# Performance work log

Hardware: AMD Instinct MI355X
Metric: run time of the kernel (lower is better)

Reference implementation:

```python
import jax, jax.numpy as jnp
import numpy as np

N_LAYERS = 2
D_MODEL = 1024
D_INNER = 2 * D_MODEL
D_STATE = 16
D_CONV = 4
DT_RANK = D_MODEL // 16  # 64
B_SZ, L = 1, 2048
EPS = 1e-5


def layernorm(x, w, b):
    mu = jnp.mean(x, axis=-1, keepdims=True)
    var = jnp.mean(jnp.square(x - mu), axis=-1, keepdims=True)
    return (x - mu) * jax.lax.rsqrt(var + EPS) * w + b


def mamba(x, in_w, cw, cb, xp_w, dtp_w, dtp_b, A_log, Dp, out_w):
    # x: [B, L, D_MODEL]
    Bn, Ln, _ = x.shape
    xz = jnp.einsum('bld,ed->ble', x, in_w)          # [B,L,2*D_INNER]
    xc, z = jnp.split(xz, 2, axis=-1)
    # causal depthwise conv1d (kernel D_CONV)
    xp = jnp.pad(xc, ((0, 0), (D_CONV - 1, 0), (0, 0)))
    xc = sum(xp[:, k:k + Ln, :] * cw[:, k] for k in range(D_CONV)) + cb
    xc = jax.nn.silu(xc)
    dbl = jnp.einsum('ble,re->blr', xc, xp_w)        # [B,L,DT_RANK+2*D_STATE]
    dt, Bm, Cm = jnp.split(dbl, [DT_RANK, DT_RANK + D_STATE], axis=-1)
    dt = jax.nn.softplus(jnp.einsum('blr,er->ble', dt, dtp_w) + dtp_b)  # [B,L,E]
    A = -jnp.exp(A_log)                              # [E,N], strictly negative
    dA = jnp.exp(dt[..., None] * A)                  # [B,L,E,N]
    dBu = (dt * xc)[..., None] * Bm[:, :, None, :]   # [B,L,E,N]

    def step(h, inp):
        dA_t, dBu_t, C_t = inp
        h = dA_t * h + dBu_t                         # [B,E,N]
        y = jnp.einsum('ben,bn->be', h, C_t)
        return h, y

    h0 = jnp.zeros((Bn, D_INNER, D_STATE), dA.dtype)
    _, ys = jax.lax.scan(step, h0, (dA.transpose(1, 0, 2, 3),
                                    dBu.transpose(1, 0, 2, 3),
                                    Cm.transpose(1, 0, 2)))
    y = ys.transpose(1, 0, 2) + xc * Dp              # [B,L,E]
    y = y * jax.nn.silu(z)
    return jnp.einsum('ble,de->bld', y, out_w)       # [B,L,D_MODEL]


def setup_inputs() -> dict:
    key = jax.random.key(0)
    ks = jax.random.split(key, 12)
    s = 0.02
    dt_init = np.log(np.expm1(0.01)).astype(np.float32)  # softplus^-1(0.01)
    A_row = jnp.log(jnp.arange(1, D_STATE + 1, dtype=jnp.float32))
    return {
        'x': jax.random.normal(ks[0], (B_SZ, L, D_MODEL), jnp.float32),
        'ln_w': jnp.ones((N_LAYERS, D_MODEL), jnp.float32),
        'ln_b': jnp.zeros((N_LAYERS, D_MODEL), jnp.float32),
        'in_proj_w': jax.random.normal(ks[1], (N_LAYERS, 2 * D_INNER, D_MODEL)) * s,
        'conv_w': jax.random.normal(ks[2], (N_LAYERS, D_INNER, D_CONV)) * 0.2,
        'conv_b': jnp.zeros((N_LAYERS, D_INNER), jnp.float32),
        'x_proj_w': jax.random.normal(ks[3], (N_LAYERS, DT_RANK + 2 * D_STATE, D_INNER)) * s,
        'dt_proj_w': jax.random.normal(ks[4], (N_LAYERS, D_INNER, DT_RANK)) * (DT_RANK ** -0.5),
        'dt_proj_b': jnp.full((N_LAYERS, D_INNER), dt_init),
        'A_log': jnp.broadcast_to(A_row, (N_LAYERS, D_INNER, D_STATE)).copy(),
        'D_skip': jnp.ones((N_LAYERS, D_INNER), jnp.float32),
        'out_proj_w': jax.random.normal(ks[5], (N_LAYERS, D_MODEL, D_INNER)) * s,
        'norm_f_w': jnp.ones((D_MODEL,), jnp.float32),
        'norm_f_b': jnp.zeros((D_MODEL,), jnp.float32),
    }


def reference(x, ln_w, ln_b, in_proj_w, conv_w, conv_b, x_proj_w, dt_proj_w,
              dt_proj_b, A_log, D_skip, out_proj_w, norm_f_w, norm_f_b):
    for i in range(N_LAYERS):
        h = layernorm(x, ln_w[i], ln_b[i])
        h = mamba(h, in_proj_w[i], conv_w[i], conv_b[i], x_proj_w[i],
                  dt_proj_w[i], dt_proj_b[i], A_log[i], D_skip[i], out_proj_w[i])
        x = h + x  # residual (dropout/drop_path are identity in eval)
    return layernorm(x, norm_f_w, norm_f_b)
```

## Files before the change

kernel.cpp:

```cpp
#include <hip/hip_runtime.h>
#include <hip/hip_bf16.h>
#include <math.h>

#define LSEQ 2048
#define DMODEL 1024
#define DINNER 2048
#define DSTATE 16
#define DCONV 4
#define DTRANK 64
#define RPROJ 96

#define CHUNK 32
#define NCHUNK (LSEQ / CHUNK)

#define XSPLIT 4

typedef __attribute__((ext_vector_type(8))) short bf16x8;
typedef __attribute__((ext_vector_type(4))) float f32x4;

__device__ __forceinline__ float softplusf(float x) {
    return (x > 20.f) ? x : log1pf(__expf(x));
}
__device__ __forceinline__ float siluf(float x) {
    return x / (1.f + __expf(-x));
}
__device__ __forceinline__ short f2bf(float f) {
    union { float f; unsigned u; } v; v.f = f;
    unsigned r = v.u + 0x7FFFu + ((v.u >> 16) & 1u);
    return (short)(r >> 16);
}
__device__ __forceinline__ float bf2f(short h) {
    union { unsigned u; float f; } v;
    v.u = ((unsigned)(unsigned short)h) << 16;
    return v.f;
}

__device__ __forceinline__ void cvt8(const float* __restrict__ s,
                                     short* __restrict__ d, int i) {
    const float4 a = *(const float4*)(s + i);
    const float4 b = *(const float4*)(s + i + 4);
    alignas(16) short h[8];
    h[0] = f2bf(a.x); h[1] = f2bf(a.y); h[2] = f2bf(a.z); h[3] = f2bf(a.w);
    h[4] = f2bf(b.x); h[5] = f2bf(b.y); h[6] = f2bf(b.z); h[7] = f2bf(b.w);
    *(uint4*)(d + i) = *(const uint4*)h;
}

__device__ __forceinline__ void ln_phase(
    const float* __restrict__ x, const float* __restrict__ w,
    const float* __restrict__ b, float* __restrict__ outf,
    short* __restrict__ outb, int bid, int tid)
{
    const int wv = tid >> 6, lane = tid & 63;
    const int row = bid * 4 + wv;
    const float* xr = x + (size_t)row * DMODEL;
    float v[16];
    float s = 0.f, sq = 0.f;
#pragma unroll
    for (int k = 0; k < 16; k++) {
        v[k] = xr[k * 64 + lane];
        s += v[k];
        sq += v[k] * v[k];
    }
#pragma unroll
    for (int off = 32; off > 0; off >>= 1) {
        s += __shfl_xor(s, off, 64);
        sq += __shfl_xor(sq, off, 64);
    }
    const float mu = s * (1.f / DMODEL);
    const float var = sq * (1.f / DMODEL) - mu * mu;
    const float rstd = rsqrtf(var + 1e-5f);
#pragma unroll
    for (int k = 0; k < 16; k++) {
        const int i = k * 64 + lane;
        const float o = (v[k] - mu) * rstd * w[i] + b[i];
        if (outf) outf[(size_t)row * DMODEL + i] = o;
        else      outb[(size_t)row * DMODEL + i] = f2bf(o);
    }
}

__global__ __launch_bounds__(256) void cvt_ln_kernel(
    const float* __restrict__ in_w, short* __restrict__ in_w_bf,
    const float* __restrict__ xp_w, short* __restrict__ xp_w_bf,
    const float* __restrict__ out_w, short* __restrict__ out_w_bf,
    const float* __restrict__ dtp_w, short* __restrict__ dtp_w_bf,
    const float* __restrict__ x_in, const float* __restrict__ ln_w,
    const float* __restrict__ ln_b, short* __restrict__ h_bf)
{
    const int n1 = 2 * (2 * DINNER) * DMODEL;
    const int n2 = 2 * RPROJ * DINNER;
    const int n3 = 2 * DMODEL * DINNER;
    const int bid = blockIdx.x;
    const int tid = threadIdx.x;
    {
        int i = (bid * 256 + tid) * 8;
        if (i < n1) { cvt8(in_w, in_w_bf, i); goto done_cvt; }
        i -= n1;
        if (i < n2) { cvt8(xp_w, xp_w_bf, i); goto done_cvt; }
        i -= n2;
        if (i < n3) { cvt8(out_w, out_w_bf, i); goto done_cvt; }
        i -= n3;
        cvt8(dtp_w, dtp_w_bf, i);
    }
done_cvt:
    if (bid < LSEQ / 4)
        ln_phase(x_in, ln_w, ln_b, nullptr, h_bf, bid, tid);
}

__global__ __launch_bounds__(256) void ln_g(
    const float* __restrict__ x, const float* __restrict__ w,
    const float* __restrict__ b, float* __restrict__ outf,
    short* __restrict__ outb)
{
    ln_phase(x, w, b, outf, outb, blockIdx.x, threadIdx.x);
}

template<int MI, int NJ, int MODE>
__global__ __launch_bounds__(256) void gemm_g(
    const short* __restrict__ A, int lda,
    const short* __restrict__ W, int ldw,
    float* __restrict__ Cf, short* __restrict__ Cb, int ldc,
    int N, int K, const float* __restrict__ resid)
{
    constexpr int BM = 32 * MI;
    constexpr int BN = 32 * NJ;
    constexpr int AISS = BM / 32;
    constexpr int WISS = BN / 32;
    __shared__ alignas(16) short As[BM * 64];
    __shared__ alignas(16) short Ws[BN * 64];

    const int tid = threadIdx.x;
    const int lane = tid & 63;
    const int w = tid >> 6;
    const int wr = w >> 1, wc = w & 1;
    const int row0 = blockIdx.y * BM;
    const int col0 = blockIdx.x * BN;
    const int kbeg = blockIdx.z * K;

    const int srow = tid >> 3;
    const int dch  = tid & 7;
    const int skch = (dch ^ (srow & 7)) * 8;

    f32x4 acc[MI][NJ];
#pragma unroll
    for (int i = 0; i < MI; i++)
#pragma unroll
        for (int j = 0; j < NJ; j++) acc[i][j] = (f32x4)0.f;

    const int lrow = lane & 15;
    const int q = lane >> 4;

    for (int kt = kbeg; kt < kbeg + K; kt += 64) {
        __syncthreads();
#pragma unroll
        for (int j = 0; j < AISS; j++) {
            const short* gp = A + (size_t)(row0 + j * 32 + srow) * lda + kt + skch;
            __builtin_amdgcn_global_load_lds(
                (const __attribute__((address_space(1))) void*)gp,
                (__attribute__((address_space(3))) void*)(&As[j * 2048 + tid * 8]),
                16, 0, 0);
        }
#pragma unroll
        for (int j = 0; j < WISS; j++) {
            const int wrow = col0 + j * 32 + srow;
            if (wrow < N) {
                const short* gp = W + (size_t)wrow * ldw + kt + skch;
                __builtin_amdgcn_global_load_lds(
                    (const __attribute__((address_space(1))) void*)gp,
                    (__attribute__((address_space(3))) void*)(&Ws[j * 2048 + tid * 8]),
                    16, 0, 0);
            }
        }
        __syncthreads();

#pragma unroll
        for (int ks = 0; ks < 2; ks++) {
            bf16x8 af[MI], bfr[NJ];
#pragma unroll
            for (int i = 0; i < MI; i++) {
                const int R = wr * (16 * MI) + i * 16 + lrow;
                const int pc = (ks * 4 + q) ^ (R & 7);
                af[i] = *(const bf16x8*)&As[R * 64 + pc * 8];
            }
#pragma unroll
            for (int j = 0; j < NJ; j++) {
                const int R = wc * (16 * NJ) + j * 16 + lrow;
                const int pc = (ks * 4 + q) ^ (R & 7);
                bfr[j] = *(const bf16x8*)&Ws[R * 64 + pc * 8];
            }
#pragma unroll
            for (int i = 0; i < MI; i++)
#pragma unroll
                for (int j = 0; j < NJ; j++)
                    acc[i][j] = __builtin_amdgcn_mfma_f32_16x16x32_bf16(
                        af[i], bfr[j], acc[i][j], 0, 0, 0);
        }
    }

    const int rbase = row0 + wr * (16 * MI);
    const int cbase = col0 + wc * (16 * NJ);
#pragma unroll
    for (int i = 0; i < MI; i++) {
#pragma unroll
        for (int j = 0; j < NJ; j++) {
            const int gcol = cbase + j * 16 + lrow;
            if (gcol < N) {
#pragma unroll
                for (int r = 0; r < 4; r++) {
                    const int grow = rbase + i * 16 + (lane >> 4) * 4 + r;
                    float v = acc[i][j][r];
                    if (MODE == 2) {
                        Cf[(size_t)grow * ldc + gcol] =
                            v + resid[(size_t)grow * ldc + gcol];
                    } else if (MODE == 3) {
                        Cb[(size_t)grow * ldc + gcol] = f2bf(v);
                    } else {
                        atomicAdd(&Cf[(size_t)grow * ldc + gcol], v);
                    }
                }
            }
        }
    }
}

__global__ __launch_bounds__(256) void dtproj_g(
    const float* __restrict__ dbl,
    const short* __restrict__ dtp_w,
    const float* __restrict__ dtp_b,
    short* __restrict__ dt_bf)
{
    __shared__ alignas(16) short As[64 * 32];
    __shared__ alignas(16) short Ws[128 * 32];
    const int tid = threadIdx.x;
    const int lane = tid & 63;
    const int w = tid >> 6;
    const int wr = w >> 1, wc = w & 1;
    const int row0 = blockIdx.y * 64;
    const int col0 = blockIdx.x * 128;
    const int srow = tid >> 2;
    const int skch = ((tid & 3) ^ ((srow >> 1) & 3)) * 8;
    const int lrow = lane & 15;
    const int q = lane >> 4;

    f32x4 acc[2][4];
#pragma unroll
    for (int i = 0; i < 2; i++)
#pragma unroll
        for (int j = 0; j < 4; j++) acc[i][j] = (f32x4)0.f;

#pragma unroll
    for (int kt = 0; kt < 64; kt += 32) {
        __syncthreads();
        {
            const float* gp = dbl + (size_t)(row0 + srow) * RPROJ + kt + skch;
            const float4 a = *(const float4*)gp;
            const float4 b = *(const float4*)(gp + 4);
            alignas(16) short h[8];
            h[0] = f2bf(a.x); h[1] = f2bf(a.y); h[2] = f2bf(a.z); h[3] = f2bf(a.w);
            h[4] = f2bf(b.x); h[5] = f2bf(b.y); h[6] = f2bf(b.z); h[7] = f2bf(b.w);
            *(uint4*)(As + tid * 8) = *(const uint4*)h;
        }
#pragma unroll
        for (int j = 0; j < 2; j++) {
            const short* gp = dtp_w + (size_t)(col0 + j * 64 + srow) * DTRANK + kt + skch;
            __builtin_amdgcn_global_load_lds(
                (const __attribute__((address_space(1))) void*)gp,
                (__attribute__((address_space(3))) void*)(&Ws[j * 2048 + tid * 8]),
                16, 0, 0);
        }
        __syncthreads();

        bf16x8 af[2], bfr[4];
#pragma unroll
        for (int i = 0; i < 2; i++) {
            const int R = wr * 32 + i * 16 + lrow;
            af[i] = *(const bf16x8*)&As[R * 32 + ((q ^ ((R >> 1) & 3)) * 8)];
        }
#pragma unroll
        for (int j = 0; j < 4; j++) {
            const int R = wc * 64 + j * 16 + lrow;
            bfr[j] = *(const bf16x8*)&Ws[R * 32 + ((q ^ ((R >> 1) & 3)) * 8)];
        }
#pragma unroll
        for (int i = 0; i < 2; i++)
#pragma unroll
            for (int j = 0; j < 4; j++)
                acc[i][j] = __builtin_amdgcn_mfma_f32_16x16x32_bf16(
                    af[i], bfr[j], acc[i][j], 0, 0, 0);
    }

    const int rbase = row0 + wr * 32;
    const int cbase = col0 + wc * 64;
#pragma unroll
    for (int i = 0; i < 2; i++)
#pragma unroll
        for (int j = 0; j < 4; j++) {
            const int gcol = cbase + j * 16 + lrow;
#pragma unroll
            for (int r = 0; r < 4; r++) {
                const int grow = rbase + i * 16 + (lane >> 4) * 4 + r;
                dt_bf[(size_t)grow * DINNER + gcol] =
                    f2bf(softplusf(acc[i][j][r] + dtp_b[gcol]));
            }
        }
}

__global__ __launch_bounds__(256) void conv_g(
    const short* __restrict__ xzb, const float* __restrict__ cw,
    const float* __restrict__ cb, short* __restrict__ xcb,
    float* __restrict__ dbl_zero)
{
    const int g = blockIdx.x * 256 + threadIdx.x;
    if (g < (LSEQ * RPROJ) / 4)
        *(float4*)(dbl_zero + g * 4) = make_float4(0.f, 0.f, 0.f, 0.f);
    const int t = g >> 8;
    const int c0 = (g & 255) * 8;
    float acc[8];
#pragma unroll
    for (int j = 0; j < 8; j++) acc[j] = cb[c0 + j];
#pragma unroll
    for (int k = 0; k < DCONV; k++) {
        const int tt = t - (DCONV - 1) + k;
        if (tt >= 0) {
            const bf16x8 v = *(const bf16x8*)(xzb + (size_t)tt * (2 * DINNER) + c0);
#pragma unroll
            for (int j = 0; j < 8; j++)
                acc[j] += bf2f(v[j]) * cw[(c0 + j) * DCONV + k];
        }
    }
    alignas(16) short h[8];
#pragma unroll
    for (int j = 0; j < 8; j++) h[j] = f2bf(siluf(acc[j]));
    *(uint4*)(xcb + (size_t)t * DINNER + c0) = *(const uint4*)h;
}

__global__ __launch_bounds__(256) void scan1_g(
    const short* __restrict__ dtb,
    const short* __restrict__ xcb,
    const float* __restrict__ dbl,
    const float* __restrict__ A_log,
    float* __restrict__ S,
    float* __restrict__ sumdt)
{
    const int e = blockIdx.x * 256 + threadIdx.x;
    const int c = blockIdx.y;
    float a[DSTATE];
#pragma unroll
    for (int n = 0; n < DSTATE; n++) a[n] = -__expf(A_log[(size_t)e * DSTATE + n]);
    float h[DSTATE];
#pragma unroll
    for (int n = 0; n < DSTATE; n++) h[n] = 0.f;
    float sd = 0.f;

    __shared__ float sBC[CHUNK][32];
    for (int i = threadIdx.x; i < CHUNK * 32; i += 256) {
        const int tl = i >> 5, j = i & 31;
        sBC[tl][j] = dbl[(size_t)(c * CHUNK + tl) * RPROJ + DTRANK + j];
    }
    __syncthreads();

    const size_t rb = (size_t)c * CHUNK * DINNER + e;
    short dt_c = dtb[rb], xc_c = xcb[rb];
#pragma unroll 4
    for (int tl = 0; tl < CHUNK; tl++) {
        short dt_n = 0, xc_n = 0;
        if (tl + 1 < CHUNK) {
            dt_n = dtb[rb + (size_t)(tl + 1) * DINNER];
            xc_n = xcb[rb + (size_t)(tl + 1) * DINNER];
        }
        const float dtv = bf2f(dt_c);
        const float du = dtv * bf2f(xc_c);
        sd += dtv;
#pragma unroll
        for (int n = 0; n < DSTATE; n++) {
            const float dA = __expf(dtv * a[n]);
            h[n] = dA * h[n] + du * sBC[tl][n];
        }
        dt_c = dt_n; xc_c = xc_n;
    }
    sumdt[(size_t)c * DINNER + e] = sd;
#pragma unroll
    for (int n = 0; n < DSTATE; n++)
        S[((size_t)c * DSTATE + n) * DINNER + e] = h[n];
}

__global__ __launch_bounds__(256) void scan2_g(
    const float* __restrict__ A_log,
    const float* __restrict__ sumdt,
    float* __restrict__ S)
{
    const int idx = blockIdx.x * 256 + threadIdx.x;
    const int e = idx & (DINNER - 1);
    const int n = idx >> 11;
    const float a = -__expf(A_log[(size_t)e * DSTATE + n]);
    const size_t base = (size_t)n * DINNER + e;
    const size_t cstr = (size_t)DSTATE * DINNER;
    float H = 0.f;
    for (int c = 0; c < NCHUNK; c += 4) {
        const float sc0 = S[base + (size_t)(c + 0) * cstr];
        const float sc1 = S[base + (size_t)(c + 1) * cstr];
        const float sc2 = S[base + (size_t)(c + 2) * cstr];
        const float sc3 = S[base + (size_t)(c + 3) * cstr];
        const float sd0 = sumdt[(size_t)(c + 0) * DINNER + e];
        const float sd1 = sumdt[(size_t)(c + 1) * DINNER + e];
        const float sd2 = sumdt[(size_t)(c + 2) * DINNER + e];
        const float sd3 = sumdt[(size_t)(c + 3) * DINNER + e];
        S[base + (size_t)(c + 0) * cstr] = H;
        H = __expf(a * sd0) * H + sc0;
        S[base + (size_t)(c + 1) * cstr] = H;
        H = __expf(a * sd1) * H + sc1;
        S[base + (size_t)(c + 2) * cstr] = H;
        H = __expf(a * sd2) * H + sc2;
        S[base + (size_t)(c + 3) * cstr] = H;
        H = __expf(a * sd3) * H + sc3;
    }
}

__global__ __launch_bounds__(256) void scan3_g(
    const short* __restrict__ dtb,
    const short* __restrict__ xcb,
    const float* __restrict__ dbl,
    const short* __restrict__ xzb,
    const float* __restrict__ A_log,
    const float* __restrict__ Dp,
    const float* __restrict__ S,
    short* __restrict__ yb)
{
    const int e = blockIdx.x * 256 + threadIdx.x;
    const int c = blockIdx.y;
    float a[DSTATE];
#pragma unroll
    for (int n = 0; n < DSTATE; n++) a[n] = -__expf(A_log[(size_t)e * DSTATE + n]);
    float h[DSTATE];
#pragma unroll
    for (int n = 0; n < DSTATE; n++)
        h[n] = S[((size_t)c * DSTATE + n) * DINNER + e];
    const float dskip = Dp[e];

    __shared__ float sBC[CHUNK][32];
    for (int i = threadIdx.x; i < CHUNK * 32; i += 256) {
        const int tl = i >> 5, j = i & 31;
        sBC[tl][j] = dbl[(size_t)(c * CHUNK + tl) * RPROJ + DTRANK + j];
    }
    __syncthreads();

    const size_t rb = (size_t)c * CHUNK * DINNER + e;
    const size_t zb = (size_t)c * CHUNK * (2 * DINNER) + DINNER + e;
    short dt_c = dtb[rb], xc_c = xcb[rb], z_c = xzb[zb];
#pragma unroll 4
    for (int tl = 0; tl < CHUNK; tl++) {
        short dt_n = 0, xc_n = 0, z_n = 0;
        if (tl + 1 < CHUNK) {
            dt_n = dtb[rb + (size_t)(tl + 1) * DINNER];
            xc_n = xcb[rb + (size_t)(tl + 1) * DINNER];
            z_n = xzb[zb + (size_t)(tl + 1) * (2 * DINNER)];
        }
        const float dtv = bf2f(dt_c);
        const float xcv = bf2f(xc_c);
        const float du = dtv * xcv;
        float yv = 0.f;
#pragma unroll
        for (int n = 0; n < DSTATE; n++) {
            const float dA = __expf(dtv * a[n]);
            h[n] = dA * h[n] + du * sBC[tl][n];
            yv += h[n] * sBC[tl][16 + n];
        }
        yv = (yv + xcv * dskip) * siluf(bf2f(z_c));
        yb[rb + (size_t)tl * DINNER] = f2bf(yv);
        dt_c = dt_n; xc_c = xc_n; z_c = z_n;
    }
}

extern "C" void kernel_launch(void* const* d_in, const int* in_sizes, int n_in,
                              void* d_out, int out_size, void* d_ws, size_t ws_size,
                              hipStream_t stream) {
    const float* x_in   = (const float*)d_in[0];
    const float* ln_w   = (const float*)d_in[1];
    const float* ln_b   = (const float*)d_in[2];
    const float* in_w   = (const float*)d_in[3];
    const float* conv_w = (const float*)d_in[4];
    const float* conv_b = (const float*)d_in[5];
    const float* xp_w   = (const float*)d_in[6];
    const float* dtp_w  = (const float*)d_in[7];
    const float* dtp_b  = (const float*)d_in[8];
    const float* A_log  = (const float*)d_in[9];
    const float* D_skip = (const float*)d_in[10];
    const float* out_w  = (const float*)d_in[11];
    const float* nf_w   = (const float*)d_in[12];
    const float* nf_b   = (const float*)d_in[13];
    float* out = (float*)d_out;

    float* w = (float*)d_ws;
    float* buf_x = w; w += (size_t)LSEQ * DMODEL;
    float* dbl   = w; w += (size_t)LSEQ * RPROJ;
    float* Sbuf  = w; w += (size_t)NCHUNK * DSTATE * DINNER;
    float* sumdt = w; w += (size_t)NCHUNK * DINNER;
    short* h_bf    = (short*)w; w += (size_t)LSEQ * DMODEL / 2;
    short* xz_bf   = (short*)w; w += (size_t)LSEQ * 2 * DINNER / 2;
    short* xc_bf   = (short*)w; w += (size_t)LSEQ * DINNER / 2;
    short* dt_bf   = (short*)w; w += (size_t)LSEQ * DINNER / 2;
    short* y_bf    = (short*)w; w += (size_t)LSEQ * DINNER / 2;
    short* in_w_bf  = (short*)w; w += (size_t)2 * (2 * DINNER) * DMODEL / 2;
    short* xp_w_bf  = (short*)w; w += (size_t)2 * RPROJ * DINNER / 2;
    short* dtp_w_bf = (short*)w; w += (size_t)2 * DINNER * DTRANK / 2;
    short* out_w_bf = (short*)w; w += (size_t)2 * DMODEL * DINNER / 2;

    {
        const int total = 2 * (2 * DINNER) * DMODEL + 2 * RPROJ * DINNER
                        + 2 * DMODEL * DINNER + 2 * DINNER * DTRANK;
        cvt_ln_kernel<<<dim3(total / (256 * 8)), dim3(256), 0, stream>>>(
            in_w, in_w_bf, xp_w, xp_w_bf, out_w, out_w_bf, dtp_w, dtp_w_bf,
            x_in, ln_w, ln_b, h_bf);
    }

    for (int layer = 0; layer < 2; layer++) {
        const float* resid_src = (layer == 0) ? x_in : buf_x;
        if (layer > 0)
            ln_g<<<dim3(LSEQ / 4), dim3(256), 0, stream>>>(
                resid_src, ln_w + layer * DMODEL, ln_b + layer * DMODEL,
                nullptr, h_bf);
        gemm_g<4, 4, 3><<<dim3((2 * DINNER) / 128, LSEQ / 128), dim3(256), 0, stream>>>(
            h_bf, DMODEL, in_w_bf + (size_t)layer * 2 * DINNER * DMODEL, DMODEL,
            nullptr, xz_bf, 2 * DINNER, 2 * DINNER, DMODEL, nullptr);
        conv_g<<<dim3((LSEQ * DINNER / 8) / 256), dim3(256), 0, stream>>>(
            xz_bf, conv_w + (size_t)layer * DINNER * DCONV, conv_b + layer * DINNER,
            xc_bf, dbl);
        gemm_g<2, 2, 6><<<dim3(2, LSEQ / 64, XSPLIT), dim3(256), 0, stream>>>(
            xc_bf, DINNER, xp_w_bf + (size_t)layer * RPROJ * DINNER, DINNER,
            dbl, nullptr, RPROJ, RPROJ, DINNER / XSPLIT, nullptr);
        dtproj_g<<<dim3(DINNER / 128, LSEQ / 64), dim3(256), 0, stream>>>(
            dbl, dtp_w_bf + (size_t)layer * DINNER * DTRANK,
            dtp_b + layer * DINNER, dt_bf);
        const float* Al = A_log + (size_t)layer * DINNER * DSTATE;
        scan1_g<<<dim3(DINNER / 256, NCHUNK), dim3(256), 0, stream>>>(
            dt_bf, xc_bf, dbl, Al, Sbuf, sumdt);
        scan2_g<<<dim3((DINNER * DSTATE) / 256), dim3(256), 0, stream>>>(
            Al, sumdt, Sbuf);
        scan3_g<<<dim3(DINNER / 256, NCHUNK), dim3(256), 0, stream>>>(
            dt_bf, xc_bf, dbl, xz_bf, Al, D_skip + layer * DINNER, Sbuf, y_bf);
        gemm_g<4, 2, 2><<<dim3(DMODEL / 64, LSEQ / 128), dim3(256), 0, stream>>>(
            y_bf, DINNER, out_w_bf + (size_t)layer * DMODEL * DINNER, DINNER,
            buf_x, nullptr, DMODEL, DMODEL, DINNER, resid_src);
    }
    ln_g<<<dim3(LSEQ / 4), dim3(256), 0, stream>>>(buf_x, nf_w, nf_b, out, nullptr);
}
```

Baseline: 476.1 us.

## Fuse causal conv+SiLU into x_proj GEMM and scans, drop xc buffer

Removes the standalone conv kernel and the xc_bf intermediate. The conv+SiLU is recomputed on the fly while staging the A tile of a new split-K x_proj GEMM, and again in both scan kernels from a sliding window over xz. Zeroing of the dbl accumulator moves into the in_proj GEMM epilogue, and CHUNK drops from 32 to 16, doubling scan parallelism at the cost of a larger chunk-state pass. The trade is redundant conv arithmetic and an extra kernel argument path in exchange for one fewer launch and less global traffic.

```diff
diff --git a/kernel.cpp b/kernel.cpp
--- a/kernel.cpp
+++ b/kernel.cpp
@@ -10,10 +10,11 @@
 #define DTRANK 64
 #define RPROJ 96
 
-#define CHUNK 32
+#define CHUNK 16
 #define NCHUNK (LSEQ / CHUNK)
 
 #define XSPLIT 4
+#define XKS (DINNER / XSPLIT)
 
 typedef __attribute__((ext_vector_type(8))) short bf16x8;
 typedef __attribute__((ext_vector_type(4))) float f32x4;
@@ -119,7 +120,8 @@
     const short* __restrict__ A, int lda,
     const short* __restrict__ W, int ldw,
     float* __restrict__ Cf, short* __restrict__ Cb, int ldc,
-    int N, int K, const float* __restrict__ resid)
+    int N, int K, const float* __restrict__ resid,
+    float* __restrict__ zbuf, int zcount4)
 {
     constexpr int BM = 32 * MI;
     constexpr int BN = 32 * NJ;
@@ -134,7 +136,6 @@
     const int wr = w >> 1, wc = w & 1;
     const int row0 = blockIdx.y * BM;
     const int col0 = blockIdx.x * BN;
-    const int kbeg = blockIdx.z * K;
 
     const int srow = tid >> 3;
     const int dch  = tid & 7;
@@ -149,7 +150,7 @@
     const int lrow = lane & 15;
     const int q = lane >> 4;
 
-    for (int kt = kbeg; kt < kbeg + K; kt += 64) {
+    for (int kt = 0; kt < K; kt += 64) {
         __syncthreads();
 #pragma unroll
         for (int j = 0; j < AISS; j++) {
@@ -211,15 +212,136 @@
                     if (MODE == 2) {
                         Cf[(size_t)grow * ldc + gcol] =
                             v + resid[(size_t)grow * ldc + gcol];
-                    } else if (MODE == 3) {
+                    } else {
                         Cb[(size_t)grow * ldc + gcol] = f2bf(v);
-                    } else {
-                        atomicAdd(&Cf[(size_t)grow * ldc + gcol], v);
                     }
                 }
             }
         }
     }
+    if (zbuf) {
+        const int g = (blockIdx.y * gridDim.x + blockIdx.x) * 256 + tid;
+        if (g < zcount4)
+            *(float4*)(zbuf + (size_t)g * 4) = make_float4(0.f, 0.f, 0.f, 0.f);
+    }
+}
+
+__global__ __launch_bounds__(256) void xproj_conv_g(
+    const short* __restrict__ xzb,
+    const float* __restrict__ cw,
+    const float* __restrict__ cb,
+    const short* __restrict__ W,
+    float* __restrict__ dbl)
+{
+    __shared__ alignas(16) short As[64 * 64];
+    __shared__ alignas(16) short Ws[64 * 64];
+    __shared__ float cw4[XKS][4];
+    __shared__ float cbl[XKS];
+
+    const int tid = threadIdx.x;
+    const int lane = tid & 63;
+    const int w = tid >> 6;
+    const int wr = w >> 1, wc = w & 1;
+    const int row0 = blockIdx.y * 64;
+    const int col0 = blockIdx.x * 64;
+    const int kbeg = blockIdx.z * XKS;
+    const int srow = tid >> 3;
+    const int dch  = tid & 7;
+    const int skch = (dch ^ (srow & 7)) * 8;
+    const int lrow = lane & 15;
+    const int q = lane >> 4;
+
+    {
+        const float4* cwsrc = (const float4*)cw;
+        *(float4*)&cw4[tid * 2][0]     = cwsrc[kbeg + tid * 2];
+        *(float4*)&cw4[tid * 2 + 1][0] = cwsrc[kbeg + tid * 2 + 1];
+        cbl[tid]       = cb[kbeg + tid];
+        cbl[tid + 256] = cb[kbeg + tid + 256];
+    }
+
+    f32x4 acc[2][2];
+#pragma unroll
+    for (int i = 0; i < 2; i++)
+#pragma unroll
+        for (int j = 0; j < 2; j++) acc[i][j] = (f32x4)0.f;
+
+    for (int kt = kbeg; kt < kbeg + XKS; kt += 64) {
+        __syncthreads();
+#pragma unroll
+        for (int j = 0; j < 2; j++) {
+            const int t = row0 + j * 32 + srow;
+            const int ch0 = kt + skch;
+            const int lc = ch0 - kbeg;
+            float a8[8];
+#pragma unroll
+            for (int i = 0; i < 8; i++) a8[i] = cbl[lc + i];
+#pragma unroll
+            for (int k = 0; k < DCONV; k++) {
+                const int tt = t - (DCONV - 1) + k;
+                if (tt >= 0) {
+                    const bf16x8 v = *(const bf16x8*)(xzb + (size_t)tt * (2 * DINNER) + ch0);
+#pragma unroll
+                    for (int i = 0; i < 8; i++)
+                        a8[i] += bf2f(v[i]) * cw4[lc + i][k];
+                }
+            }
+            alignas(16) short h8[8];
+#pragma unroll
+            for (int i = 0; i < 8; i++) h8[i] = f2bf(siluf(a8[i]));
+            *(uint4*)(&As[j * 2048 + tid * 8]) = *(const uint4*)h8;
+        }
+#pragma unroll
+        for (int j = 0; j < 2; j++) {
+            const int wrow = col0 + j * 32 + srow;
+            if (wrow < RPROJ) {
+                const short* gp = W + (size_t)wrow * DINNER + kt + skch;
+                __builtin_amdgcn_global_load_lds(
+                    (const __attribute__((address_space(1))) void*)gp,
+                    (__attribute__((address_space(3))) void*)(&Ws[j * 2048 + tid * 8]),
+                    16, 0, 0);
+            }
+        }
+        __syncthreads();
+
+#pragma unroll
+        for (int ks = 0; ks < 2; ks++) {
+            bf16x8 af[2], bfr[2];
+#pragma unroll
+            for (int i = 0; i < 2; i++) {
+                const int R = wr * 32 + i * 16 + lrow;
+                const int pc = (ks * 4 + q) ^ (R & 7);
+                af[i] = *(const bf16x8*)&As[R * 64 + pc * 8];
+            }
+#pragma unroll
+            for (int j = 0; j < 2; j++) {
+                const int R = wc * 32 + j * 16 + lrow;
+                const int pc = (ks * 4 + q) ^ (R & 7);
+                bfr[j] = *(const bf16x8*)&Ws[R * 64 + pc * 8];
+            }
+#pragma unroll
+            for (int i = 0; i < 2; i++)
+#pragma unroll
+                for (int j = 0; j < 2; j++)
+                    acc[i][j] = __builtin_amdgcn_mfma_f32_16x16x32_bf16(
+                        af[i], bfr[j], acc[i][j], 0, 0, 0);
+        }
+    }
+
+    const int rbase = row0 + wr * 32;
+    const int cbase = col0 + wc * 32;
+#pragma unroll
+    for (int i = 0; i < 2; i++)
+#pragma unroll
+        for (int j = 0; j < 2; j++) {
+            const int gcol = cbase + j * 16 + lrow;
+            if (gcol < RPROJ) {
+#pragma unroll
+                for (int r = 0; r < 4; r++) {
+                    const int grow = rbase + i * 16 + (lane >> 4) * 4 + r;
+                    atomicAdd(&dbl[(size_t)grow * RPROJ + gcol], acc[i][j][r]);
+                }
+            }
+        }
 }
 
 __global__ __launch_bounds__(256) void dtproj_g(
@@ -304,38 +426,11 @@
         }
 }
 
-__global__ __launch_bounds__(256) void conv_g(
-    const short* __restrict__ xzb, const float* __restrict__ cw,
-    const float* __restrict__ cb, short* __restrict__ xcb,
-    float* __restrict__ dbl_zero)
-{
-    const int g = blockIdx.x * 256 + threadIdx.x;
-    if (g < (LSEQ * RPROJ) / 4)
-        *(float4*)(dbl_zero + g * 4) = make_float4(0.f, 0.f, 0.f, 0.f);
-    const int t = g >> 8;
-    const int c0 = (g & 255) * 8;
-    float acc[8];
-#pragma unroll
-    for (int j = 0; j < 8; j++) acc[j] = cb[c0 + j];
-#pragma unroll
-    for (int k = 0; k < DCONV; k++) {
-        const int tt = t - (DCONV - 1) + k;
-        if (tt >= 0) {
-            const bf16x8 v = *(const bf16x8*)(xzb + (size_t)tt * (2 * DINNER) + c0);
-#pragma unroll
-            for (int j = 0; j < 8; j++)
-                acc[j] += bf2f(v[j]) * cw[(c0 + j) * DCONV + k];
-        }
-    }
-    alignas(16) short h[8];
-#pragma unroll
-    for (int j = 0; j < 8; j++) h[j] = f2bf(siluf(acc[j]));
-    *(uint4*)(xcb + (size_t)t * DINNER + c0) = *(const uint4*)h;
-}
-
 __global__ __launch_bounds__(256) void scan1_g(
     const short* __restrict__ dtb,
-    const short* __restrict__ xcb,
+    const short* __restrict__ xzb,
+    const float* __restrict__ cw,
+    const float* __restrict__ cb,
     const float* __restrict__ dbl,
     const float* __restrict__ A_log,
     float* __restrict__ S,
@@ -358,24 +453,35 @@
     }
     __syncthreads();
 
+    const float4 cwv = *(const float4*)(cw + (size_t)e * 4);
+    const float cbv = cb[e];
     const size_t rb = (size_t)c * CHUNK * DINNER + e;
-    short dt_c = dtb[rb], xc_c = xcb[rb];
-#pragma unroll 4
+    const size_t xzr = (size_t)c * CHUNK * (2 * DINNER) + e;
+    float w1 = 0.f, w2 = 0.f, w3 = 0.f;
+    if (c > 0) {
+        w1 = bf2f(xzb[xzr - 1 * (2 * DINNER)]);
+        w2 = bf2f(xzb[xzr - 2 * (2 * DINNER)]);
+        w3 = bf2f(xzb[xzr - 3 * (2 * DINNER)]);
+    }
+    float w0 = bf2f(xzb[xzr]);
+    short dt_c = dtb[rb];
+#pragma unroll
     for (int tl = 0; tl < CHUNK; tl++) {
-        short dt_n = 0, xc_n = 0;
+        short dt_n = 0; float xz_n = 0.f;
         if (tl + 1 < CHUNK) {
             dt_n = dtb[rb + (size_t)(tl + 1) * DINNER];
-            xc_n = xcb[rb + (size_t)(tl + 1) * DINNER];
-        }
+            xz_n = bf2f(xzb[xzr + (size_t)(tl + 1) * (2 * DINNER)]);
+        }
+        const float xcv = siluf(cbv + cwv.x * w3 + cwv.y * w2 + cwv.z * w1 + cwv.w * w0);
         const float dtv = bf2f(dt_c);
-        const float du = dtv * bf2f(xc_c);
+        const float du = dtv * xcv;
         sd += dtv;
 #pragma unroll
         for (int n = 0; n < DSTATE; n++) {
             const float dA = __expf(dtv * a[n]);
             h[n] = dA * h[n] + du * sBC[tl][n];
         }
-        dt_c = dt_n; xc_c = xc_n;
+        w3 = w2; w2 = w1; w1 = w0; w0 = xz_n; dt_c = dt_n;
     }
     sumdt[(size_t)c * DINNER + e] = sd;
 #pragma unroll
@@ -417,9 +523,10 @@
 
 __global__ __launch_bounds__(256) void scan3_g(
     const short* __restrict__ dtb,
-    const short* __restrict__ xcb,
+    const short* __restrict__ xzb,
+    const float* __restrict__ cw,
+    const float* __restrict__ cb,
     const float* __restrict__ dbl,
-    const short* __restrict__ xzb,
     const float* __restrict__ A_log,
     const float* __restrict__ Dp,
     const float* __restrict__ S,
@@ -443,19 +550,29 @@
     }
     __syncthreads();
 
+    const float4 cwv = *(const float4*)(cw + (size_t)e * 4);
+    const float cbv = cb[e];
     const size_t rb = (size_t)c * CHUNK * DINNER + e;
-    const size_t zb = (size_t)c * CHUNK * (2 * DINNER) + DINNER + e;
-    short dt_c = dtb[rb], xc_c = xcb[rb], z_c = xzb[zb];
-#pragma unroll 4
+    const size_t xzr = (size_t)c * CHUNK * (2 * DINNER) + e;
+    const size_t zb = xzr + DINNER;
+    float w1 = 0.f, w2 = 0.f, w3 = 0.f;
+    if (c > 0) {
+        w1 = bf2f(xzb[xzr - 1 * (2 * DINNER)]);
+        w2 = bf2f(xzb[xzr - 2 * (2 * DINNER)]);
+        w3 = bf2f(xzb[xzr - 3 * (2 * DINNER)]);
+    }
+    float w0 = bf2f(xzb[xzr]);
+    short dt_c = dtb[rb], z_c = xzb[zb];
+#pragma unroll
     for (int tl = 0; tl < CHUNK; tl++) {
-        short dt_n = 0, xc_n = 0, z_n = 0;
+        short dt_n = 0, z_n = 0; float xz_n = 0.f;
         if (tl + 1 < CHUNK) {
             dt_n = dtb[rb + (size_t)(tl + 1) * DINNER];
-            xc_n = xcb[rb + (size_t)(tl + 1) * DINNER];
+            xz_n = bf2f(xzb[xzr + (size_t)(tl + 1) * (2 * DINNER)]);
             z_n = xzb[zb + (size_t)(tl + 1) * (2 * DINNER)];
         }
+        const float xcv = siluf(cbv + cwv.x * w3 + cwv.y * w2 + cwv.z * w1 + cwv.w * w0);
         const float dtv = bf2f(dt_c);
-        const float xcv = bf2f(xc_c);
         const float du = dtv * xcv;
         float yv = 0.f;
 #pragma unroll
@@ -466,7 +583,7 @@
         }
         yv = (yv + xcv * dskip) * siluf(bf2f(z_c));
         yb[rb + (size_t)tl * DINNER] = f2bf(yv);
-        dt_c = dt_n; xc_c = xc_n; z_c = z_n;
+        w3 = w2; w2 = w1; w1 = w0; w0 = xz_n; dt_c = dt_n; z_c = z_n;
     }
 }
 
@@ -496,7 +613,6 @@
     float* sumdt = w; w += (size_t)NCHUNK * DINNER;
     short* h_bf    = (short*)w; w += (size_t)LSEQ * DMODEL / 2;
     short* xz_bf   = (short*)w; w += (size_t)LSEQ * 2 * DINNER / 2;
-    short* xc_bf   = (short*)w; w += (size_t)LSEQ * DINNER / 2;
     short* dt_bf   = (short*)w; w += (size_t)LSEQ * DINNER / 2;
     short* y_bf    = (short*)w; w += (size_t)LSEQ * DINNER / 2;
     short* in_w_bf  = (short*)w; w += (size_t)2 * (2 * DINNER) * DMODEL / 2;
@@ -514,32 +630,32 @@
 
     for (int layer = 0; layer < 2; layer++) {
         const float* resid_src = (layer == 0) ? x_in : buf_x;
+        const float* cwl = conv_w + (size_t)layer * DINNER * DCONV;
+        const float* cbl = conv_b + (size_t)layer * DINNER;
         if (layer > 0)
             ln_g<<<dim3(LSEQ / 4), dim3(256), 0, stream>>>(
                 resid_src, ln_w + layer * DMODEL, ln_b + layer * DMODEL,
                 nullptr, h_bf);
         gemm_g<4, 4, 3><<<dim3((2 * DINNER) / 128, LSEQ / 128), dim3(256), 0, stream>>>(
             h_bf, DMODEL, in_w_bf + (size_t)layer * 2 * DINNER * DMODEL, DMODEL,
-            nullptr, xz_bf, 2 * DINNER, 2 * DINNER, DMODEL, nullptr);
-        conv_g<<<dim3((LSEQ * DINNER / 8) / 256), dim3(256), 0, stream>>>(
-            xz_bf, conv_w + (size_t)layer * DINNER * DCONV, conv_b + layer * DINNER,
-            xc_bf, dbl);
-        gemm_g<2, 2, 6><<<dim3(2, LSEQ / 64, XSPLIT), dim3(256), 0, stream>>>(
-            xc_bf, DINNER, xp_w_bf + (size_t)layer * RPROJ * DINNER, DINNER,
-            dbl, nullptr, RPROJ, RPROJ, DINNER / XSPLIT, nullptr);
+            nullptr, xz_bf, 2 * DINNER, 2 * DINNER, DMODEL, nullptr,
+            dbl, (LSEQ * RPROJ) / 4);
+        xproj_conv_g<<<dim3(2, LSEQ / 64, XSPLIT), dim3(256), 0, stream>>>(
+            xz_bf, cwl, cbl, xp_w_bf + (size_t)layer * RPROJ * DINNER, dbl);
         dtproj_g<<<dim3(DINNER / 128, LSEQ / 64), dim3(256), 0, stream>>>(
             dbl, dtp_w_bf + (size_t)layer * DINNER * DTRANK,
             dtp_b + layer * DINNER, dt_bf);
         const float* Al = A_log + (size_t)layer * DINNER * DSTATE;
         scan1_g<<<dim3(DINNER / 256, NCHUNK), dim3(256), 0, stream>>>(
-            dt_bf, xc_bf, dbl, Al, Sbuf, sumdt);
+            dt_bf, xz_bf, cwl, cbl, dbl, Al, Sbuf, sumdt);
         scan2_g<<<dim3((DINNER * DSTATE) / 256), dim3(256), 0, stream>>>(
             Al, sumdt, Sbuf);
         scan3_g<<<dim3(DINNER / 256, NCHUNK), dim3(256), 0, stream>>>(
-            dt_bf, xc_bf, dbl, xz_bf, Al, D_skip + layer * DINNER, Sbuf, y_bf);
+            dt_bf, xz_bf, cwl, cbl, dbl, Al, D_skip + layer * DINNER, Sbuf, y_bf);
         gemm_g<4, 2, 2><<<dim3(DMODEL / 64, LSEQ / 128), dim3(256), 0, stream>>>(
             y_bf, DINNER, out_w_bf + (size_t)layer * DMODEL * DINNER, DINNER,
-            buf_x, nullptr, DMODEL, DMODEL, DINNER, resid_src);
+            buf_x, nullptr, DMODEL, DMODEL, DINNER, resid_src,
+            nullptr, 0);
     }
     ln_g<<<dim3(LSEQ / 4), dim3(256), 0, stream>>>(buf_x, nf_w, nf_b, out, nullptr);
 }
```

After: 457.8 us. -3.8%, faster.
